# Kernel tuning notes

Measured on AMD Instinct MI355X. Metric: run time of the kernel, lower is better.

## Reference

```python
import jax, jax.numpy as jnp
import numpy as np

B, S, D = 64, 2048, 512


def setup_inputs() -> dict:
    key = jax.random.key(0)
    k1, k2, k3, k4 = jax.random.split(key, 4)
    decoder_output = jax.random.normal(k1, (B, 1, D), dtype=jnp.float32)
    encoder_output = jax.random.normal(k2, (B, S, D), dtype=jnp.float32)
    # W_a_tanh: Dense(D) applied to concat([dec, enc]) of width 2D
    scale_w = 1.0 / np.sqrt(2 * D)
    W_t = jax.random.normal(k3, (2 * D, D), dtype=jnp.float32) * scale_w
    b_t = jnp.zeros((D,), dtype=jnp.float32)
    # v_a: Dense(1)
    v_a = jax.random.normal(k4, (D, 1), dtype=jnp.float32) * (1.0 / np.sqrt(D))
    b_v = jnp.zeros((1,), dtype=jnp.float32)
    return {
        "decoder_output": decoder_output,
        "encoder_output": encoder_output,
        "W_t": W_t,
        "b_t": b_t,
        "v_a": v_a,
        "b_v": b_v,
    }


def reference(decoder_output, encoder_output, W_t, b_t, v_a, b_v):
    # concat-variant Luong attention
    dec = jnp.broadcast_to(decoder_output, encoder_output.shape)       # [B,S,D]
    concated = jnp.concatenate((dec, encoder_output), axis=-1)          # [B,S,2D]
    hidden = jnp.tanh(jnp.einsum('bse,ed->bsd', concated, W_t) + b_t)   # [B,S,D]
    score = (jnp.einsum('bsd,do->bso', hidden, v_a) + b_v)              # [B,S,1]
    score = jnp.transpose(score, (0, 2, 1))                             # [B,1,S]
    alignment_vector = jax.nn.softmax(score, axis=2)                    # [B,1,S]
    context_vector = jnp.matmul(alignment_vector, encoder_output)       # [B,1,D]
    return (context_vector, alignment_vector)
```

## Files before the change

kernel.cpp:

```cpp
#include <hip/hip_runtime.h>

#define BB 64
#define SS 2048
#define DD 512

typedef __attribute__((ext_vector_type(8))) short bf16x8;
typedef __attribute__((ext_vector_type(4))) float f32x4;

__device__ __forceinline__ unsigned f2bf(float f) {
    unsigned u = __float_as_uint(f);
    u += 0x7FFFu + ((u >> 16) & 1u);
    return u >> 16;
}

__device__ __forceinline__ float fast_tanh(float x) {
    float ax = fabsf(x);
    float e = __expf(-2.0f * ax);
    float t = (1.0f - e) * __builtin_amdgcn_rcpf(1.0f + e);
    return x < 0.0f ? -t : t;
}

__global__ void prep_w(const float* __restrict__ W, short* __restrict__ Bt) {
    __shared__ float tile[64][65];
    int kt = blockIdx.x >> 3;
    int nt = blockIdx.x & 7;
    int t = threadIdx.x;
    int c = t & 63;
    int rbase = (t >> 6) * 16;
    #pragma unroll
    for (int i = 0; i < 16; ++i) {
        int r = rbase + i;
        tile[r][c] = W[(size_t)(512 + kt * 64 + r) * DD + nt * 64 + c];
    }
    __syncthreads();
    #pragma unroll
    for (int i = 0; i < 16; ++i) {
        int r = rbase + i;
        Bt[(size_t)(nt * 64 + r) * DD + kt * 64 + c] = (short)f2bf(tile[c][r]);
    }
}

__global__ void prep_p(const float* __restrict__ dec, const float* __restrict__ W,
                       const float* __restrict__ bt, float* __restrict__ p) {
    int b = blockIdx.x;
    int d = blockIdx.y * 256 + threadIdx.x;
    float acc = bt[d];
    const float* dv = dec + (size_t)b * DD;
    #pragma unroll 8
    for (int e = 0; e < DD; ++e)
        acc += dv[e] * W[(size_t)e * DD + d];
    p[(size_t)b * DD + d] = acc;
}

__global__ __launch_bounds__(1024, 4)
void fused_k(const float* __restrict__ enc, const short* __restrict__ Bt,
             const float* __restrict__ p, const float* __restrict__ va,
             float* __restrict__ score, float* __restrict__ ml,
             float* __restrict__ pctx) {
    __shared__ char smem[65536 + 2048 + 256];
    char* AhiB = smem;
    float (*red)[512] = (float (*)[512])smem;
    float (*sp)[32]   = (float (*)[32])(smem + 65536);
    float* elds       = (float*)(smem + 67584);

    const int tid  = threadIdx.x;
    const int wave = tid >> 6;
    const int lane = tid & 63;
    const int lm   = lane & 15;
    const int lq   = lane >> 4;
    const int wm   = wave >> 3;
    const int wn   = wave & 7;
    const int blk  = blockIdx.x;
    const int b    = blk >> 5;
    const size_t m0 = (size_t)blk * 64;

    const int srow = tid >> 4;
    const int sc   = tid & 15;
    const unsigned srowB = (unsigned)srow * 1024u;
    const unsigned swsr  = (unsigned)(srow & 7) << 4;
    const float* aptr = enc + (m0 + (size_t)srow) * DD + sc * 2;

    const unsigned swlm = (unsigned)(lm & 7) << 4;
    const unsigned arow0 = (unsigned)(wm * 32 + lm) * 1024u;
    const unsigned arow1 = arow0 + 16u * 1024u;
    const short* Bw = Bt + (size_t)(wn * 64 + lm) * DD + lq * 8;

    f32x4 acc[2][4];
    #pragma unroll
    for (int i = 0; i < 2; ++i)
        #pragma unroll
        for (int j = 0; j < 4; ++j)
            acc[i][j] = (f32x4){0.f, 0.f, 0.f, 0.f};

    float2 stg[4];
    stg[0] = *(const float2*)(aptr);
    stg[1] = *(const float2*)(aptr + 32);
    stg[2] = *(const float2*)(aptr + 64);
    {
        unsigned hv = f2bf(stg[0].x) | (f2bf(stg[0].y) << 16);
        *(unsigned*)(AhiB + (srowB + (((unsigned)sc * 4u) ^ swsr))) = hv;
    }
    __syncthreads();

    #pragma unroll
    for (int kt = 0; kt < 16; ++kt) {
        if (kt < 13)
            stg[(kt + 3) & 3] = *(const float2*)(aptr + (kt + 3) * 32);

        const unsigned kb = (unsigned)kt * 64u;
        bf16x8 af0 = *(const bf16x8*)(AhiB + arow0 + ((kb + lq * 16u) ^ swlm));
        bf16x8 af1 = *(const bf16x8*)(AhiB + arow1 + ((kb + lq * 16u) ^ swlm));

        #pragma unroll
        for (int nf = 0; nf < 4; ++nf) {
            bf16x8 bfr = *(const bf16x8*)(Bw + nf * 16 * DD + kt * 32);
            acc[0][nf] = __builtin_amdgcn_mfma_f32_16x16x32_bf16(af0, bfr, acc[0][nf], 0, 0, 0);
            acc[1][nf] = __builtin_amdgcn_mfma_f32_16x16x32_bf16(af1, bfr, acc[1][nf], 0, 0, 0);
        }

        if (kt < 15) {
            float2 x = stg[(kt + 1) & 3];
            unsigned hv = f2bf(x.x) | (f2bf(x.y) << 16);
            *(unsigned*)(AhiB + (srowB + (((unsigned)((kt + 1) * 64) + sc * 4u) ^ swsr))) = hv;
        }
        __syncthreads();
    }

    const float* pb = p + (size_t)b * DD;
    float rowsum[2][4];
    #pragma unroll
    for (int mf = 0; mf < 2; ++mf)
        #pragma unroll
        for (int r = 0; r < 4; ++r) rowsum[mf][r] = 0.f;

    #pragma unroll
    for (int nf = 0; nf < 4; ++nf) {
        int n = wn * 64 + nf * 16 + lm;
        float pv = pb[n];
        float vv = va[n];
        #pragma unroll
        for (int mf = 0; mf < 2; ++mf)
            #pragma unroll
            for (int r = 0; r < 4; ++r)
                rowsum[mf][r] += fast_tanh(pv + acc[mf][nf][r]) * vv;
    }
    #pragma unroll
    for (int mf = 0; mf < 2; ++mf)
        #pragma unroll
        for (int r = 0; r < 4; ++r) {
            float s = rowsum[mf][r];
            s += __shfl_xor(s, 1);
            s += __shfl_xor(s, 2);
            s += __shfl_xor(s, 4);
            s += __shfl_xor(s, 8);
            rowsum[mf][r] = s;
        }
    if (lm == 0) {
        #pragma unroll
        for (int mf = 0; mf < 2; ++mf)
            #pragma unroll
            for (int r = 0; r < 4; ++r)
                sp[wave][mf * 16 + lq * 4 + r] = rowsum[mf][r];
    }
    __syncthreads();

    if (tid < 64) {
        const int base = (tid >> 5) * 8;
        const int rl = tid & 31;
        float s = 0.f;
        #pragma unroll
        for (int w = 0; w < 8; ++w) s += sp[base + w][rl];
        score[m0 + tid] = s;
        float mx = s;
        #pragma unroll
        for (int off = 32; off > 0; off >>= 1) mx = fmaxf(mx, __shfl_xor(mx, off));
        float e = __expf(s - mx);
        float l = e;
        #pragma unroll
        for (int off = 32; off > 0; off >>= 1) l += __shfl_xor(l, off);
        elds[tid] = e;
        if (tid == 0) {
            ml[(size_t)blk * 2]     = mx;
            ml[(size_t)blk * 2 + 1] = l;
        }
    }
    __syncthreads();

    {
        const int d = tid & 511;
        const int g = tid >> 9;
        const float* erow = enc + (m0 + (size_t)g * 32) * DD + d;
        float v = 0.f;
        #pragma unroll
        for (int s = 0; s < 32; ++s)
            v += elds[g * 32 + s] * erow[(size_t)s * DD];
        red[g][d] = v;
    }
    __syncthreads();
    if (tid < 512)
        pctx[(size_t)blk * 512 + tid] = red[0][tid] + red[1][tid];
}

__global__ void combine_k(const float* __restrict__ score, const float* __restrict__ ml,
                          const float* __restrict__ pctx, float* __restrict__ ctx,
                          float* __restrict__ align) {
    __shared__ float sc[32];
    __shared__ float MB, LB;
    const int b = blockIdx.x, tid = threadIdx.x;
    if (tid < 32) sc[tid] = ml[(size_t)(b * 32 + tid) * 2];
    __syncthreads();
    if (tid == 0) {
        float M = sc[0];
        #pragma unroll
        for (int i = 1; i < 32; ++i) M = fmaxf(M, sc[i]);
        float L = 0.f;
        for (int i = 0; i < 32; ++i) {
            float w = __expf(sc[i] - M);
            L += w * ml[(size_t)(b * 32 + i) * 2 + 1];
            sc[i] = w;
        }
        MB = M;
        LB = L;
    }
    __syncthreads();
    const float M = MB, Linv = 1.0f / LB;
    float a0 = 0.f, a1 = 0.f;
    for (int i = 0; i < 32; ++i) {
        float w = sc[i];
        const float* pc = pctx + (size_t)(b * 32 + i) * 512;
        a0 += w * pc[tid];
        a1 += w * pc[tid + 256];
    }
    ctx[(size_t)b * DD + tid]       = a0 * Linv;
    ctx[(size_t)b * DD + tid + 256] = a1 * Linv;
    const float* sr = score + (size_t)b * SS;
    float* al = align + (size_t)b * SS;
    #pragma unroll
    for (int i = 0; i < 8; ++i) {
        int s = i * 256 + tid;
        al[s] = __expf(sr[s] - M) * Linv;
    }
}

extern "C" void kernel_launch(void* const* d_in, const int* in_sizes, int n_in,
                              void* d_out, int out_size, void* d_ws, size_t ws_size,
                              hipStream_t stream) {
    const float* dec = (const float*)d_in[0];
    const float* enc = (const float*)d_in[1];
    const float* W   = (const float*)d_in[2];
    const float* bt  = (const float*)d_in[3];
    const float* va  = (const float*)d_in[4];

    float* out   = (float*)d_out;
    float* ctx   = out;
    float* align = out + BB * DD;

    char*  ws    = (char*)d_ws;
    short* Bt    = (short*)ws;
    float* p     = (float*)(ws + 524288);
    float* score = (float*)(ws + 655360);
    float* ml    = (float*)(ws + 1179648);
    float* pctx  = (float*)(ws + 1196032);

    prep_w<<<64, 256, 0, stream>>>(W, Bt);
    prep_p<<<dim3(BB, 2), 256, 0, stream>>>(dec, W, bt, p);
    fused_k<<<BB * 32, 1024, 0, stream>>>(enc, Bt, p, va, score, ml, pctx);
    combine_k<<<BB, 256, 0, stream>>>(score, ml, pctx, ctx, align);
}
```

Measured before the change: 654.8 us.

## Halve fused block tile to 32 rows and double-buffer B fragments in registers

```diff
diff --git a/kernel.cpp b/kernel.cpp
--- a/kernel.cpp
+++ b/kernel.cpp
@@ -52,27 +52,24 @@
     p[(size_t)b * DD + d] = acc;
 }
 
-__global__ __launch_bounds__(1024, 4)
+__global__ __launch_bounds__(512, 4)
 void fused_k(const float* __restrict__ enc, const short* __restrict__ Bt,
              const float* __restrict__ p, const float* __restrict__ va,
              float* __restrict__ score, float* __restrict__ ml,
              float* __restrict__ pctx) {
-    __shared__ char smem[65536 + 2048 + 256];
+    __shared__ char smem[32768 + 1024 + 128];
     char* AhiB = smem;
-    float (*red)[512] = (float (*)[512])smem;
-    float (*sp)[32]   = (float (*)[32])(smem + 65536);
-    float* elds       = (float*)(smem + 67584);
+    float (*sp)[32] = (float (*)[32])(smem + 32768);
+    float* elds     = (float*)(smem + 33792);
 
     const int tid  = threadIdx.x;
     const int wave = tid >> 6;
     const int lane = tid & 63;
     const int lm   = lane & 15;
     const int lq   = lane >> 4;
-    const int wm   = wave >> 3;
-    const int wn   = wave & 7;
     const int blk  = blockIdx.x;
-    const int b    = blk >> 5;
-    const size_t m0 = (size_t)blk * 64;
+    const int b    = blk >> 6;
+    const size_t m0 = (size_t)blk * 32;
 
     const int srow = tid >> 4;
     const int sc   = tid & 15;
@@ -81,9 +78,9 @@
     const float* aptr = enc + (m0 + (size_t)srow) * DD + sc * 2;
 
     const unsigned swlm = (unsigned)(lm & 7) << 4;
-    const unsigned arow0 = (unsigned)(wm * 32 + lm) * 1024u;
+    const unsigned arow0 = (unsigned)lm * 1024u;
     const unsigned arow1 = arow0 + 16u * 1024u;
-    const short* Bw = Bt + (size_t)(wn * 64 + lm) * DD + lq * 8;
+    const short* Bw = Bt + (size_t)(wave * 64 + lm) * DD + lq * 8;
 
     f32x4 acc[2][4];
     #pragma unroll
@@ -91,6 +88,11 @@
         #pragma unroll
         for (int j = 0; j < 4; ++j)
             acc[i][j] = (f32x4){0.f, 0.f, 0.f, 0.f};
+
+    bf16x8 bb[2][4];
+    #pragma unroll
+    for (int nf = 0; nf < 4; ++nf)
+        bb[0][nf] = *(const bf16x8*)(Bw + nf * 16 * DD);
 
     float2 stg[4];
     stg[0] = *(const float2*)(aptr);
@@ -104,6 +106,11 @@
 
     #pragma unroll
     for (int kt = 0; kt < 16; ++kt) {
+        const int cur = kt & 1;
+        if (kt < 15)
+            #pragma unroll
+            for (int nf = 0; nf < 4; ++nf)
+                bb[cur ^ 1][nf] = *(const bf16x8*)(Bw + nf * 16 * DD + (kt + 1) * 32);
         if (kt < 13)
             stg[(kt + 3) & 3] = *(const float2*)(aptr + (kt + 3) * 32);
 
@@ -113,9 +120,8 @@
 
         #pragma unroll
         for (int nf = 0; nf < 4; ++nf) {
-            bf16x8 bfr = *(const bf16x8*)(Bw + nf * 16 * DD + kt * 32);
-            acc[0][nf] = __builtin_amdgcn_mfma_f32_16x16x32_bf16(af0, bfr, acc[0][nf], 0, 0, 0);
-            acc[1][nf] = __builtin_amdgcn_mfma_f32_16x16x32_bf16(af1, bfr, acc[1][nf], 0, 0, 0);
+            acc[0][nf] = __builtin_amdgcn_mfma_f32_16x16x32_bf16(af0, bb[cur][nf], acc[0][nf], 0, 0, 0);
+            acc[1][nf] = __builtin_amdgcn_mfma_f32_16x16x32_bf16(af1, bb[cur][nf], acc[1][nf], 0, 0, 0);
         }
 
         if (kt < 15) {
@@ -135,7 +141,7 @@
 
     #pragma unroll
     for (int nf = 0; nf < 4; ++nf) {
-        int n = wn * 64 + nf * 16 + lm;
+        int n = wave * 64 + nf * 16 + lm;
         float pv = pb[n];
         float vv = va[n];
         #pragma unroll
@@ -164,20 +170,18 @@
     }
     __syncthreads();
 
-    if (tid < 64) {
-        const int base = (tid >> 5) * 8;
-        const int rl = tid & 31;
+    if (tid < 32) {
         float s = 0.f;
         #pragma unroll
-        for (int w = 0; w < 8; ++w) s += sp[base + w][rl];
+        for (int w = 0; w < 8; ++w) s += sp[w][tid];
         score[m0 + tid] = s;
         float mx = s;
         #pragma unroll
-        for (int off = 32; off > 0; off >>= 1) mx = fmaxf(mx, __shfl_xor(mx, off));
+        for (int off = 16; off > 0; off >>= 1) mx = fmaxf(mx, __shfl_xor(mx, off));
         float e = __expf(s - mx);
         float l = e;
         #pragma unroll
-        for (int off = 32; off > 0; off >>= 1) l += __shfl_xor(l, off);
+        for (int off = 16; off > 0; off >>= 1) l += __shfl_xor(l, off);
         elds[tid] = e;
         if (tid == 0) {
             ml[(size_t)blk * 2]     = mx;
@@ -187,36 +191,31 @@
     __syncthreads();
 
     {
-        const int d = tid & 511;
-        const int g = tid >> 9;
-        const float* erow = enc + (m0 + (size_t)g * 32) * DD + d;
+        const float* erow = enc + m0 * DD + tid;
         float v = 0.f;
         #pragma unroll
         for (int s = 0; s < 32; ++s)
-            v += elds[g * 32 + s] * erow[(size_t)s * DD];
-        red[g][d] = v;
-    }
-    __syncthreads();
-    if (tid < 512)
-        pctx[(size_t)blk * 512 + tid] = red[0][tid] + red[1][tid];
+            v += elds[s] * erow[(size_t)s * DD];
+        pctx[(size_t)blk * 512 + tid] = v;
+    }
 }
 
 __global__ void combine_k(const float* __restrict__ score, const float* __restrict__ ml,
                           const float* __restrict__ pctx, float* __restrict__ ctx,
                           float* __restrict__ align) {
-    __shared__ float sc[32];
+    __shared__ float sc[64];
     __shared__ float MB, LB;
     const int b = blockIdx.x, tid = threadIdx.x;
-    if (tid < 32) sc[tid] = ml[(size_t)(b * 32 + tid) * 2];
+    if (tid < 64) sc[tid] = ml[(size_t)(b * 64 + tid) * 2];
     __syncthreads();
     if (tid == 0) {
         float M = sc[0];
         #pragma unroll
-        for (int i = 1; i < 32; ++i) M = fmaxf(M, sc[i]);
+        for (int i = 1; i < 64; ++i) M = fmaxf(M, sc[i]);
         float L = 0.f;
-        for (int i = 0; i < 32; ++i) {
+        for (int i = 0; i < 64; ++i) {
             float w = __expf(sc[i] - M);
-            L += w * ml[(size_t)(b * 32 + i) * 2 + 1];
+            L += w * ml[(size_t)(b * 64 + i) * 2 + 1];
             sc[i] = w;
         }
         MB = M;
@@ -225,9 +224,9 @@
     __syncthreads();
     const float M = MB, Linv = 1.0f / LB;
     float a0 = 0.f, a1 = 0.f;
-    for (int i = 0; i < 32; ++i) {
+    for (int i = 0; i < 64; ++i) {
         float w = sc[i];
-        const float* pc = pctx + (size_t)(b * 32 + i) * 512;
+        const float* pc = pctx + (size_t)(b * 64 + i) * 512;
         a0 += w * pc[tid];
         a1 += w * pc[tid + 256];
     }
@@ -260,10 +259,10 @@
     float* p     = (float*)(ws + 524288);
     float* score = (float*)(ws + 655360);
     float* ml    = (float*)(ws + 1179648);
-    float* pctx  = (float*)(ws + 1196032);
+    float* pctx  = (float*)(ws + 1212416);
 
     prep_w<<<64, 256, 0, stream>>>(W, Bt);
     prep_p<<<dim3(BB, 2), 256, 0, stream>>>(dec, W, bt, p);
-    fused_k<<<BB * 32, 1024, 0, stream>>>(enc, Bt, p, va, score, ml, pctx);
+    fused_k<<<BB * 64, 512, 0, stream>>>(enc, Bt, p, va, score, ml, pctx);
     combine_k<<<BB, 256, 0, stream>>>(score, ml, pctx, ctx, align);
 }
```

New measurement: 633.5 us. -3.2%, faster.
